# Kernel tuning notes

Measured on AMD Instinct MI355X. Metric: run time of the kernel, lower is better.

Reference implementation:

```python
import jax, jax.numpy as jnp
import numpy as np
from jax import lax

PAD = 1  # conv padding; with kernel 3 and stride (2,1) this preserves (D, D)


def setup_inputs() -> dict:
    key = jax.random.key(0)
    k1, k2, k3 = jax.random.split(key, 3)
    B, L, D = 16, 256, 64
    num_layer = 2
    x = jax.random.normal(k1, (B, L, D, D), dtype=jnp.float32)
    # Conv2d(in=1, out=1, kernel=3x3) per layer, stacked: (num_layer, O=1, I=1, 3, 3)
    W = jax.random.normal(k2, (num_layer, 1, 1, 3, 3), dtype=jnp.float32) * 0.1
    b = jax.random.normal(k3, (num_layer,), dtype=jnp.float32) * 0.1
    return {"x": x, "W": W, "b": b}


def _layer(x, W, b):
    # x: (B, L, D, D); W: (1, 1, 3, 3); b: scalar
    B, L, D, _ = x.shape
    xs = jnp.transpose(x, (1, 0, 2, 3))[:, :, None]  # (L, B, 1, D, D)
    h0 = jnp.zeros((B, 1, D, D), dtype=x.dtype)

    def step(h, xt):
        inp = jnp.concatenate([xt, h], axis=2)  # (B, 1, 2D, D)
        out = lax.conv_general_dilated(
            inp, W, window_strides=(2, 1),
            padding=((PAD, PAD), (PAD, PAD)),
            dimension_numbers=("NCHW", "OIHW", "NCHW"))  # (B, 1, D, D)
        h_new = jnp.tanh(out + b)
        return h_new, h_new

    _, hs = lax.scan(step, h0, xs)  # (L, B, 1, D, D)
    return jnp.transpose(hs[:, :, 0], (1, 0, 2, 3))  # (B, L, D, D)


def reference(x, W, b):
    # Stacked CnnBasedRnn layers; dropout is identity in eval mode.
    out = x
    for l in range(W.shape[0]):
        out = _layer(out, W[l], b[l])
    return out
```

## Files before the change

kernel.cpp:

```cpp
#include <hip/hip_runtime.h>
#include <math.h>

#define B_ 16
#define L_ 256
#define D_ 64

#define CHUNK 16
#define WARM  5
#define NCH   (L_ / CHUNK)

#define PITCH 64
#define NSLOT 127
#define FBUF  (NSLOT * PITCH)
#define LDSZ  (2 * FBUF)

__device__ __forceinline__ int swz(int s) { return (s + (s >> 1)) & 7; }

__device__ __forceinline__ float ftanh(float x) {
    float ax = fabsf(x);
    float e  = __builtin_amdgcn_exp2f(-2.8853900818f * ax);
    float r  = (1.0f - e) * __builtin_amdgcn_rcpf(1.0f + e);
    return copysignf(r, x);
}

__device__ __forceinline__ float dpp_shr1(float x) {
    int r = __builtin_amdgcn_update_dpp(0, __float_as_int(x), 0x138, 0xF, 0xF, true);
    return __int_as_float(r);
}
__device__ __forceinline__ float dpp_shl1(float x) {
    int r = __builtin_amdgcn_update_dpp(0, __float_as_int(x), 0x130, 0xF, 0xF, true);
    return __int_as_float(r);
}

__global__ __launch_bounds__(512, 1) void fused_layer(
        const float* __restrict__ X, float* __restrict__ H,
        const float* __restrict__ Wl, const float* __restrict__ bl) {
    __shared__ float lds[LDSZ];

    const int tid    = threadIdx.x;
    const int b      = blockIdx.x >> 4;
    const int ch     = blockIdx.x & (NCH - 1);
    const int T0     = ch * CHUNK;
    const int tw     = (T0 >= WARM) ? (T0 - WARM) : 0;
    const int tend   = T0 + CHUNK;
    const int btbase = b * L_;

    const int r   = tid >> 3;
    const int l8  = tid & 7;
    const int q0  = l8 << 1;
    const int sx  = r + 1;
    const int vx  = swz(sx);
    const int xw0 = sx * PITCH + ((q0 ^ vx) << 2);
    const int xw1 = sx * PITCH + (((q0 + 1) ^ vx) << 2);
    const int  i    = r;
    const int  ic   = (i < 63) ? i : 62;
    const int  c0   = l8 << 3;
    const int  sh   = 65 + i;
    const int  vh   = swz(sh);
    const int  hw0  = sh * PITCH + ((q0 ^ vh) << 2);
    const int  hw1  = sh * PITCH + (((q0 + 1) ^ vh) << 2);
    const bool le0  = (l8 == 0);
    const bool le7  = (l8 == 7);

    int ro0[3], ro1[3];
#pragma unroll
    for (int ki = 0; ki < 3; ++ki) {
        const int s = 2 * ic + ki;
        const int v = swz(s);
        const int sb = s * PITCH;
        ro0[ki] = sb + ((q0 ^ v) << 2);
        ro1[ki] = sb + (((q0 + 1) ^ v) << 2);
    }

    float w[9];
#pragma unroll
    for (int k = 0; k < 9; ++k) w[k] = Wl[k];
    const float bias = bl[0];
    const float4 z4 = make_float4(0.f, 0.f, 0.f, 0.f);

    for (int k = tid; k < LDSZ / 4; k += 512)
        reinterpret_cast<float4*>(lds)[k] = z4;
    __syncthreads();

    float* cur = lds;
    float* nxt = lds + FBUF;

    {
        const float* xg = X + (((size_t)(btbase + tw)) << 12) + (tid << 3);
        *reinterpret_cast<float4*>(cur + xw0) = reinterpret_cast<const float4*>(xg)[0];
        *reinterpret_cast<float4*>(cur + xw1) = reinterpret_cast<const float4*>(xg)[1];
    }
    float4 pa, pb;
    {
        const int t1 = (tw + 1 < L_) ? tw + 1 : L_ - 1;
        const float* xg = X + (((size_t)(btbase + t1)) << 12) + (tid << 3);
        pa = reinterpret_cast<const float4*>(xg)[0];
        pb = reinterpret_cast<const float4*>(xg)[1];
    }
    __syncthreads();

    for (int t = tw; t < tend; ++t) {
        const int t2 = (t + 2 < L_) ? t + 2 : L_ - 1;
        const float* xg = X + (((size_t)(btbase + t2)) << 12) + (tid << 3);
        const float4 na = reinterpret_cast<const float4*>(xg)[0];
        const float4 nb = reinterpret_cast<const float4*>(xg)[1];

        float u0[8], u1[8], u2[8];
#pragma unroll
        for (int k = 0; k < 8; ++k) { u0[k] = 0.f; u1[k] = bias; u2[k] = 0.f; }
#pragma unroll
        for (int ki = 0; ki < 3; ++ki) {
            const float4 o0 = *reinterpret_cast<const float4*>(cur + ro0[ki]);
            const float4 o1 = *reinterpret_cast<const float4*>(cur + ro1[ki]);
            const float g[8] = {o0.x, o0.y, o0.z, o0.w, o1.x, o1.y, o1.z, o1.w};
            const float wa = w[ki*3], wb = w[ki*3+1], wc = w[ki*3+2];
#pragma unroll
            for (int k = 0; k < 8; ++k) {
                u0[k] = fmaf(wa, g[k], u0[k]);
                u1[k] = fmaf(wb, g[k], u1[k]);
                u2[k] = fmaf(wc, g[k], u2[k]);
            }
        }
        const float eLr = dpp_shr1(u0[7]);
        const float eRr = dpp_shl1(u2[0]);
        const float eL  = le0 ? 0.f : eLr;
        const float eR  = le7 ? 0.f : eRr;

        float o[8];
        o[0] = ftanh(eL + u1[0] + u2[1]);
#pragma unroll
        for (int k = 1; k < 7; ++k)
            o[k] = ftanh(u0[k-1] + u1[k] + u2[k+1]);
        o[7] = ftanh(u0[6] + u1[7] + eR);

        if (i < 63 && t >= T0) {
            float* gd = H + (((size_t)(btbase + t)) << 12) + (i << 6) + c0;
            *reinterpret_cast<float4*>(gd)     = make_float4(o[0],o[1],o[2],o[3]);
            *reinterpret_cast<float4*>(gd + 4) = make_float4(o[4],o[5],o[6],o[7]);
        }
        if (i <= 61) {
            *reinterpret_cast<float4*>(nxt + hw0) = make_float4(o[0],o[1],o[2],o[3]);
            *reinterpret_cast<float4*>(nxt + hw1) = make_float4(o[4],o[5],o[6],o[7]);
        }
        {
            *reinterpret_cast<float4*>(nxt + xw0) = pa;
            *reinterpret_cast<float4*>(nxt + xw1) = pb;
        }
        __syncthreads();
        pa = na; pb = nb;
        float* tmp = cur; cur = nxt; nxt = tmp;
    }
}

#define SDEPTH 16
__global__ void scan63(float* __restrict__ dst,
                       const float* __restrict__ src,
                       const float* __restrict__ Wl,
                       const float* __restrict__ bl) {
    const int b = blockIdx.x;
    const int j = threadIdx.x;
    float w[9];
#pragma unroll
    for (int k = 0; k < 9; ++k) w[k] = Wl[k];
    const float bias = bl[0];

    const size_t ST = (size_t)D_ * D_;
    const float* s61 = src + (size_t)b * L_ * ST + 61 * 64 + j;
    const float* s62 = src + (size_t)b * L_ * ST + 62 * 64 + j;
    float*       d63 = dst + (size_t)b * L_ * ST + 63 * 64 + j;

    float s = ftanh(bias);
    d63[0] = s;

    float p61[SDEPTH], p62[SDEPTH];
#pragma unroll
    for (int u = 0; u < SDEPTH; ++u) {
        p61[u] = s61[(size_t)u * ST];
        p62[u] = s62[(size_t)u * ST];
    }

    for (int t0 = 1; t0 < 256; t0 += SDEPTH) {
#pragma unroll
        for (int u = 0; u < SDEPTH; ++u) {
            const int t = t0 + u;
            if (t > 255) break;
            const float r61 = p61[u], r62 = p62[u];
            int tp = t + SDEPTH - 1;
            if (tp > 255) tp = 255;
            p61[u] = s61[(size_t)tp * ST];
            p62[u] = s62[(size_t)tp * ST];
            float l1 = dpp_shr1(r61), q1 = dpp_shl1(r61);
            float l2 = dpp_shr1(r62), q2 = dpp_shl1(r62);
            float p = bias;
            p = fmaf(w[0], l1, p); p = fmaf(w[1], r61, p); p = fmaf(w[2], q1, p);
            p = fmaf(w[3], l2, p); p = fmaf(w[4], r62, p); p = fmaf(w[5], q2, p);
            float ls = dpp_shr1(s), rs = dpp_shl1(s);
            float z = fmaf(w[6], ls, fmaf(w[7], s, fmaf(w[8], rs, p)));
            s = ftanh(z);
            d63[(size_t)t * ST] = s;
        }
    }
}

extern "C" void kernel_launch(void* const* d_in, const int* in_sizes, int n_in,
                              void* d_out, int out_size, void* d_ws, size_t ws_size,
                              hipStream_t stream) {
    const float* x    = (const float*)d_in[0];
    const float* W    = (const float*)d_in[1];
    const float* bias = (const float*)d_in[2];
    float* out = (float*)d_out;
    float* h1  = (float*)d_ws;

    for (int l = 0; l < 2; ++l) {
        const float* X  = (l == 0) ? x  : h1;
        float*       H  = (l == 0) ? h1 : out;
        fused_layer<<<B_ * NCH, 512, 0, stream>>>(X, H, W + l * 9, bias + l);
        scan63<<<B_, 64, 0, stream>>>(H, H, W + l * 9, bias + l);
    }
}
```

Before: 118.5 us.

## Read x rows for the first half directly from global into registers, shrink LDS

Output rows 0-31 of the stride-2 conv depend only on x rows, so those threads now load their three input rows from global memory straight into registers, prefetching one step ahead. Only the hidden rows and x row 63 are staged in LDS, which halves the LDS footprint and removes the per-step cooperative staging of the whole x frame. In exchange the x rows are read redundantly by overlapping threads, half the threads take a different branch, and register pressure rises from the extra float4 buffers.

```diff
diff --git a/kernel.cpp b/kernel.cpp
--- a/kernel.cpp
+++ b/kernel.cpp
@@ -10,7 +10,7 @@
 #define NCH   (L_ / CHUNK)
 
 #define PITCH 64
-#define NSLOT 127
+#define NSLOT 63
 #define FBUF  (NSLOT * PITCH)
 #define LDSZ  (2 * FBUF)
 
@@ -48,29 +48,29 @@
     const int r   = tid >> 3;
     const int l8  = tid & 7;
     const int q0  = l8 << 1;
-    const int sx  = r + 1;
-    const int vx  = swz(sx);
-    const int xw0 = sx * PITCH + ((q0 ^ vx) << 2);
-    const int xw1 = sx * PITCH + (((q0 + 1) ^ vx) << 2);
-    const int  i    = r;
-    const int  ic   = (i < 63) ? i : 62;
-    const int  c0   = l8 << 3;
-    const int  sh   = 65 + i;
-    const int  vh   = swz(sh);
-    const int  hw0  = sh * PITCH + ((q0 ^ vh) << 2);
-    const int  hw1  = sh * PITCH + (((q0 + 1) ^ vh) << 2);
-    const bool le0  = (l8 == 0);
-    const bool le7  = (l8 == 7);
+    const int c0  = l8 << 3;
+    const bool lvl0 = (r < 32);
+    const bool st63 = (r == 63);
+    const int  rr   = (r < 62) ? r : 62;
 
     int ro0[3], ro1[3];
 #pragma unroll
     for (int ki = 0; ki < 3; ++ki) {
-        const int s = 2 * ic + ki;
-        const int v = swz(s);
-        const int sb = s * PITCH;
-        ro0[ki] = sb + ((q0 ^ v) << 2);
-        ro1[ki] = sb + (((q0 + 1) ^ v) << 2);
-    }
+        const int cr = 2 * rr - 65 + ki;
+        const int s  = (cr < 0) ? 62 : cr;
+        const int v  = swz(s);
+        ro0[ki] = s * PITCH + ((q0 ^ v) << 2);
+        ro1[ki] = s * PITCH + (((q0 + 1) ^ v) << 2);
+    }
+    const int vh  = swz(r);
+    const int hw0 = r * PITCH + ((q0 ^ vh) << 2);
+    const int hw1 = r * PITCH + (((q0 + 1) ^ vh) << 2);
+    const int v62 = swz(62);
+    const int xw0 = 62 * PITCH + ((q0 ^ v62) << 2);
+    const int xw1 = 62 * PITCH + (((q0 + 1) ^ v62) << 2);
+
+    const bool le0 = (l8 == 0);
+    const bool le7 = (l8 == 7);
 
     float w[9];
 #pragma unroll
@@ -85,34 +85,68 @@
     float* cur = lds;
     float* nxt = lds + FBUF;
 
-    {
-        const float* xg = X + (((size_t)(btbase + tw)) << 12) + (tid << 3);
-        *reinterpret_cast<float4*>(cur + xw0) = reinterpret_cast<const float4*>(xg)[0];
-        *reinterpret_cast<float4*>(cur + xw1) = reinterpret_cast<const float4*>(xg)[1];
-    }
-    float4 pa, pb;
-    {
+    float4 cx[6];
+    if (lvl0) {
+        const float* xf = X + ((size_t)(btbase + tw) << 12);
+#pragma unroll
+        for (int ki = 0; ki < 3; ++ki) {
+            const int cr = 2 * r - 1 + ki;
+            const float* rp = xf + (cr << 6) + c0;
+            const bool ok = (cr >= 0);
+            cx[ki*2]   = ok ? *reinterpret_cast<const float4*>(rp)     : z4;
+            cx[ki*2+1] = ok ? *reinterpret_cast<const float4*>(rp + 4) : z4;
+        }
+    }
+    float4 p63a = z4, p63b = z4;
+    if (st63) {
+        const float* xf = X + ((size_t)(btbase + tw) << 12) + (63 << 6) + c0;
+        *reinterpret_cast<float4*>(cur + xw0) = *reinterpret_cast<const float4*>(xf);
+        *reinterpret_cast<float4*>(cur + xw1) = *reinterpret_cast<const float4*>(xf + 4);
         const int t1 = (tw + 1 < L_) ? tw + 1 : L_ - 1;
-        const float* xg = X + (((size_t)(btbase + t1)) << 12) + (tid << 3);
-        pa = reinterpret_cast<const float4*>(xg)[0];
-        pb = reinterpret_cast<const float4*>(xg)[1];
+        const float* xn = X + ((size_t)(btbase + t1) << 12) + (63 << 6) + c0;
+        p63a = *reinterpret_cast<const float4*>(xn);
+        p63b = *reinterpret_cast<const float4*>(xn + 4);
     }
     __syncthreads();
 
     for (int t = tw; t < tend; ++t) {
-        const int t2 = (t + 2 < L_) ? t + 2 : L_ - 1;
-        const float* xg = X + (((size_t)(btbase + t2)) << 12) + (tid << 3);
-        const float4 na = reinterpret_cast<const float4*>(xg)[0];
-        const float4 nb = reinterpret_cast<const float4*>(xg)[1];
+        float4 nx[6];
+        if (lvl0) {
+            const int tn = (t + 1 < L_) ? t + 1 : L_ - 1;
+            const float* xf = X + ((size_t)(btbase + tn) << 12);
+#pragma unroll
+            for (int ki = 0; ki < 3; ++ki) {
+                const int cr = 2 * r - 1 + ki;
+                const float* rp = xf + (cr << 6) + c0;
+                const bool ok = (cr >= 0);
+                nx[ki*2]   = ok ? *reinterpret_cast<const float4*>(rp)     : z4;
+                nx[ki*2+1] = ok ? *reinterpret_cast<const float4*>(rp + 4) : z4;
+            }
+        }
+        float4 n63a, n63b;
+        if (st63) {
+            const int t2 = (t + 2 < L_) ? t + 2 : L_ - 1;
+            const float* xn = X + ((size_t)(btbase + t2) << 12) + (63 << 6) + c0;
+            n63a = *reinterpret_cast<const float4*>(xn);
+            n63b = *reinterpret_cast<const float4*>(xn + 4);
+        }
 
         float u0[8], u1[8], u2[8];
 #pragma unroll
         for (int k = 0; k < 8; ++k) { u0[k] = 0.f; u1[k] = bias; u2[k] = 0.f; }
 #pragma unroll
         for (int ki = 0; ki < 3; ++ki) {
-            const float4 o0 = *reinterpret_cast<const float4*>(cur + ro0[ki]);
-            const float4 o1 = *reinterpret_cast<const float4*>(cur + ro1[ki]);
-            const float g[8] = {o0.x, o0.y, o0.z, o0.w, o1.x, o1.y, o1.z, o1.w};
+            float g[8];
+            if (lvl0) {
+                const float4 o0 = cx[ki*2], o1 = cx[ki*2+1];
+                g[0]=o0.x; g[1]=o0.y; g[2]=o0.z; g[3]=o0.w;
+                g[4]=o1.x; g[5]=o1.y; g[6]=o1.z; g[7]=o1.w;
+            } else {
+                const float4 o0 = *reinterpret_cast<const float4*>(cur + ro0[ki]);
+                const float4 o1 = *reinterpret_cast<const float4*>(cur + ro1[ki]);
+                g[0]=o0.x; g[1]=o0.y; g[2]=o0.z; g[3]=o0.w;
+                g[4]=o1.x; g[5]=o1.y; g[6]=o1.z; g[7]=o1.w;
+            }
             const float wa = w[ki*3], wb = w[ki*3+1], wc = w[ki*3+2];
 #pragma unroll
             for (int k = 0; k < 8; ++k) {
@@ -133,21 +167,25 @@
             o[k] = ftanh(u0[k-1] + u1[k] + u2[k+1]);
         o[7] = ftanh(u0[6] + u1[7] + eR);
 
-        if (i < 63 && t >= T0) {
-            float* gd = H + (((size_t)(btbase + t)) << 12) + (i << 6) + c0;
+        if (r < 63 && t >= T0) {
+            float* gd = H + (((size_t)(btbase + t)) << 12) + (r << 6) + c0;
             *reinterpret_cast<float4*>(gd)     = make_float4(o[0],o[1],o[2],o[3]);
             *reinterpret_cast<float4*>(gd + 4) = make_float4(o[4],o[5],o[6],o[7]);
         }
-        if (i <= 61) {
+        if (r <= 61) {
             *reinterpret_cast<float4*>(nxt + hw0) = make_float4(o[0],o[1],o[2],o[3]);
             *reinterpret_cast<float4*>(nxt + hw1) = make_float4(o[4],o[5],o[6],o[7]);
         }
-        {
-            *reinterpret_cast<float4*>(nxt + xw0) = pa;
-            *reinterpret_cast<float4*>(nxt + xw1) = pb;
+        if (st63) {
+            *reinterpret_cast<float4*>(nxt + xw0) = p63a;
+            *reinterpret_cast<float4*>(nxt + xw1) = p63b;
+            p63a = n63a; p63b = n63b;
+        }
+        if (lvl0) {
+#pragma unroll
+            for (int k = 0; k < 6; ++k) cx[k] = nx[k];
         }
         __syncthreads();
-        pa = na; pb = nb;
         float* tmp = cur; cur = nxt; nxt = tmp;
     }
 }
```

Result: slower. 139.9 us (+18.0%).
